# Optimization experiments

Hardware: AMD Instinct MI355X
Metric: run time of the kernel (lower is better)

## Reference

```python
import jax, jax.numpy as jnp
import numpy as np

EPS = 1e-5  # torch GroupNorm default


def setup_inputs() -> dict:
    key = jax.random.key(0)
    ks = jax.random.split(key, 6)
    C = 256
    B, F, H, W = 1, 8, 32, 32
    scale = 1.0 / np.sqrt(C)  # keep logits well-scaled
    return {
        "x": jax.random.normal(ks[0], (B, C, F, H, W), dtype=jnp.float32),
        "gn_w": jnp.ones((C,), jnp.float32),
        "gn_b": jnp.zeros((C,), jnp.float32),
        "qw": jax.random.normal(ks[1], (C, C), jnp.float32) * scale,
        "qb": jnp.zeros((C,), jnp.float32),
        "kw": jax.random.normal(ks[2], (C, C), jnp.float32) * scale,
        "kb": jnp.zeros((C,), jnp.float32),
        "vw": jax.random.normal(ks[3], (C, C), jnp.float32) * scale,
        "vb": jnp.zeros((C,), jnp.float32),
        "ow": jax.random.normal(ks[4], (C, C), jnp.float32) * scale,
        "ob": jnp.zeros((C,), jnp.float32),
    }


def reference(x, gn_w, gn_b, qw, qb, kw, kb, vw, vb, ow, ob):
    B, C, F, H, W = x.shape
    N = F * H * W
    # GroupNorm(1, C): normalize over (C,F,H,W) per sample, per-channel affine
    mean = jnp.mean(x, axis=(1, 2, 3, 4), keepdims=True)
    var = jnp.var(x, axis=(1, 2, 3, 4), keepdims=True)
    xn = (x - mean) * jax.lax.rsqrt(var + EPS)
    xn = xn * gn_w[None, :, None, None, None] + gn_b[None, :, None, None, None]
    xf = xn.reshape(B, C, N)  # [B, C, N]
    # 1x1x1 Conv3d == channel matmul
    q = jnp.einsum('oc,bcn->bon', qw, xf) + qb[None, :, None]
    k = jnp.einsum('oc,bcn->bon', kw, xf) + kb[None, :, None]
    v = jnp.einsum('oc,bcn->bon', vw, xf) + vb[None, :, None]
    # scores[b, n_q, n_k] = q^T k, scaled by C^-0.5
    scores = jnp.einsum('bcn,bcm->bnm', q, k) * (C ** -0.5)
    weights = jax.nn.softmax(scores, axis=-1)  # over keys
    # attention[b, c, n_q] = sum_m v[b,c,m] * weights[b,n_q,m]
    att = jnp.einsum('bcm,bnm->bcn', v, weights)
    att = jnp.einsum('oc,bcn->bon', ow, att) + ob[None, :, None]
    return xn + att.reshape(B, C, F, H, W)
```

## Files before the change

### kernel.cpp

```cpp
#include <hip/hip_runtime.h>
#include <hip/hip_bf16.h>
#include <cstdint>

#define NSP 8192
#define CCH 256
#define KBLK 32
#define NSPLIT 8
#define KEYS_PER_SPLIT 1024
#define NTILES 32

typedef __attribute__((ext_vector_type(4))) float f32x4;
typedef __attribute__((ext_vector_type(16))) float f32x16;
typedef __attribute__((ext_vector_type(8))) short bf16x8;
typedef __attribute__((ext_vector_type(2))) unsigned int u32x2;

__device__ __forceinline__ ushort f2bf(float f) {
  union { float f; uint32_t u; } v; v.f = f;
  uint32_t r = (v.u + 0x7FFFu + ((v.u >> 16) & 1u)) >> 16;
  return (ushort)r;
}
__device__ __forceinline__ float bf2f(ushort u) {
  union { uint32_t u; float f; } v; v.u = ((uint32_t)u) << 16; return v.f;
}
__device__ __forceinline__ uint32_t pk2bf(float lo, float hi) {
  __hip_bfloat162 h = __float22bfloat162_rn({lo, hi});
  union { __hip_bfloat162 h; uint32_t u; } c; c.h = h; return c.u;
}

__device__ __forceinline__ void gload_lds16(const void* g, void* l) {
  auto gp = (const __attribute__((address_space(1))) uint32_t*)(uintptr_t)g;
  auto lp = (__attribute__((address_space(3))) uint32_t*)(uint32_t)(uintptr_t)l;
  __builtin_amdgcn_global_load_lds(gp, lp, 16, 0, 0);
}

__device__ __forceinline__ void perm32swap(uint32_t& a, uint32_t& b) {
#if __has_builtin(__builtin_amdgcn_permlane32_swap)
  u32x2 r = __builtin_amdgcn_permlane32_swap(a, b, false, false);
  a = r[0]; b = r[1];
#else
  uint32_t sa = __shfl_xor((int)a, 32), sb = __shfl_xor((int)b, 32);
  bool lo = (threadIdx.x & 63) < 32;
  uint32_t na = lo ? a : sb;
  uint32_t nb = lo ? sa : b;
  a = na; b = nb;
#endif
}

__global__ __launch_bounds__(256) void k_stats1(const float* __restrict__ x,
                                                float* __restrict__ part) {
  int t = threadIdx.x, b = blockIdx.x;
  float s = 0.f, ss = 0.f;
  const float4* x4 = (const float4*)x;
  for (int i = 0; i < 4; ++i) {
    float4 v = x4[(size_t)i * 131072 + b * 256 + t];
    s += v.x + v.y + v.z + v.w;
    ss += v.x * v.x + v.y * v.y + v.z * v.z + v.w * v.w;
  }
  for (int m = 1; m < 64; m <<= 1) { s += __shfl_xor(s, m); ss += __shfl_xor(ss, m); }
  __shared__ float ls[4], lss[4];
  int w = t >> 6, lane = t & 63;
  if (lane == 0) { ls[w] = s; lss[w] = ss; }
  __syncthreads();
  if (t == 0) {
    part[b * 2 + 0] = ls[0] + ls[1] + ls[2] + ls[3];
    part[b * 2 + 1] = lss[0] + lss[1] + lss[2] + lss[3];
  }
}

__global__ __launch_bounds__(256) void k_castw(const float* __restrict__ qw, const float* __restrict__ kw,
                                               const float* __restrict__ vw, const float* __restrict__ ow,
                                               ushort* __restrict__ wqkv, ushort* __restrict__ wo,
                                               const float* __restrict__ part, float* __restrict__ stat) {
  if (blockIdx.x == 1024) {
    int t = threadIdx.x;
    float s = 0.f, ss = 0.f;
    for (int i = t; i < 512; i += 256) { s += part[i * 2]; ss += part[i * 2 + 1]; }
    for (int m = 1; m < 64; m <<= 1) { s += __shfl_xor(s, m); ss += __shfl_xor(ss, m); }
    __shared__ float ls[4], lss[4];
    int w = t >> 6, lane = t & 63;
    if (lane == 0) { ls[w] = s; lss[w] = ss; }
    __syncthreads();
    if (t == 0) {
      float sum = ls[0] + ls[1] + ls[2] + ls[3];
      float ssum = lss[0] + lss[1] + lss[2] + lss[3];
      float mean = sum * (1.f / 2097152.f);
      float var = ssum * (1.f / 2097152.f) - mean * mean;
      stat[0] = mean;
      stat[1] = rsqrtf(var + 1e-5f);
    }
    return;
  }
  int idx = blockIdx.x * 256 + threadIdx.x;
  if (idx < 65536) wqkv[idx] = f2bf(qw[idx]);
  else if (idx < 131072) wqkv[idx] = f2bf(kw[idx - 65536]);
  else if (idx < 196608) wqkv[idx] = f2bf(vw[idx - 131072]);
  else wo[idx - 196608] = f2bf(ow[idx - 196608]);
}

__global__ __launch_bounds__(256) void k_norm_t(const float* __restrict__ x,
                                                const float* __restrict__ gw, const float* __restrict__ gb,
                                                const float* __restrict__ stat, ushort* __restrict__ xnT) {
  __shared__ float tile[64][66];
  int n0 = blockIdx.x * 64, c0 = blockIdx.y * 64;
  int t = threadIdx.x, colr = t & 63, rq = t >> 6;
  float mean = stat[0], rinv = stat[1];
  for (int rr = 0; rr < 16; ++rr) {
    int row = rr * 4 + rq;
    int c = c0 + row;
    float v = x[(size_t)c * NSP + n0 + colr];
    tile[row][colr] = (v - mean) * rinv * gw[c] + gb[c];
  }
  __syncthreads();
  for (int rr = 0; rr < 16; ++rr) {
    int rowW = rr * 4 + rq;
    xnT[(size_t)(n0 + rowW) * 256 + c0 + colr] = f2bf(tile[colr][rowW]);
  }
}

__global__ __launch_bounds__(256) void k_qkv(const ushort* __restrict__ xnT, const ushort* __restrict__ wqkv,
                                             const float* __restrict__ qb, const float* __restrict__ kb,
                                             const float* __restrict__ vb,
                                             ushort* __restrict__ qT, ushort* __restrict__ kT,
                                             ushort* __restrict__ v_tiles) {
  __shared__ ushort tile[64][80];
  int nb = blockIdx.x, ob = blockIdx.y;
  int w = threadIdx.x >> 6, lane = threadIdx.x & 63;
  int l16 = lane & 15, kgrp = lane >> 4;
  int n_row = nb * 64 + w * 16 + l16;
  bf16x8 a[8];
  const bf16x8* arow = (const bf16x8*)(xnT + (size_t)n_row * 256);
  for (int ks = 0; ks < 8; ++ks) a[ks] = arow[ks * 4 + kgrp];
  f32x4 acc[4];
  for (int ct = 0; ct < 4; ++ct) {
    int o = ob * 64 + ct * 16 + l16;
    const bf16x8* brow = (const bf16x8*)(wqkv + (size_t)o * 256);
    f32x4 c = {0.f, 0.f, 0.f, 0.f};
    for (int ks = 0; ks < 8; ++ks)
      c = __builtin_amdgcn_mfma_f32_16x16x32_bf16(a[ks], brow[ks * 4 + kgrp], c, 0, 0, 0);
    acc[ct] = c;
  }
  const float SCALE = 0.0625f * 1.44269504088896340736f;
  if (ob < 8) {
    for (int ct = 0; ct < 4; ++ct) {
      int o = ob * 64 + ct * 16 + l16;
      for (int r = 0; r < 4; ++r) {
        int n = nb * 64 + w * 16 + kgrp * 4 + r;
        float v = acc[ct][r];
        if (o < 256) qT[(size_t)n * 256 + o] = f2bf((v + qb[o]) * SCALE);
        else kT[(size_t)n * 256 + (o - 256)] = f2bf(v + kb[o - 256]);
      }
    }
  } else {
    for (int ct = 0; ct < 4; ++ct) {
      int o_l = ct * 16 + l16;
      for (int r = 0; r < 4; ++r) {
        int n_l = w * 16 + kgrp * 4 + r;
        tile[o_l][n_l] = f2bf(acc[ct][r] + vb[(ob - 8) * 64 + o_l]);
      }
    }
    __syncthreads();
    for (int j = 0; j < 2; ++j) {
      int idx = j * 256 + threadIdx.x;
      int tile_l = idx >> 8, slot = (idx >> 6) & 3, c_l = idx & 63;
      size_t off = (size_t)(nb * 2 + tile_l) * 8192 + slot * 2048 +
                   (size_t)((ob - 8) * 64 + c_l) * 8;
      *(uint4*)((char*)v_tiles + off * 2) = *(const uint4*)&tile[c_l][tile_l * 32 + slot * 8];
    }
  }
}

__global__ __launch_bounds__(512, 2) void k_attn(const ushort* __restrict__ qT, const ushort* __restrict__ kT,
                                                 const ushort* __restrict__ v_tiles,
                                                 ushort* __restrict__ Opart, float* __restrict__ mpart,
                                                 float* __restrict__ lpart) {
  __shared__ __align__(16) ushort SMEM[32768];
  ushort* k_lds = SMEM;
  ushort* v_lds = SMEM + 16384;

  int bid = blockIdx.x;
  int split = bid & 7, qblk = bid >> 3;
  int t = threadIdx.x, w = t >> 6, lane = t & 63;
  int l31 = lane & 31, lhi = lane >> 5, l7 = lane & 7;
  int q0w = qblk * 256 + w * 32;

  bf16x8 qf[16];
  {
    const char* qbase = (const char*)qT + (size_t)(q0w + l31) * 512;
#pragma unroll
    for (int cs = 0; cs < 16; ++cs)
      qf[cs] = *(const bf16x8*)(qbase + cs * 32 + lhi * 16);
  }

  f32x16 acc[8] = {};
  float m_r = -1e30f, l_p = 0.f;

  const char* kT_b = (const char*)kT + (size_t)split * KEYS_PER_SPLIT * 512;
  const char* v_b = (const char*)v_tiles + (size_t)split * KEYS_PER_SPLIT * 512;

  auto STAGE = [&](int tt, int bsel) {
    const char* ksrc = kT_b + (size_t)tt * KBLK * 512;
    char* kdst = (char*)(k_lds + bsel * 8192) + w * 2048;
#pragma unroll
    for (int i = 0; i < 2; ++i) {
      int keyloc = w * 4 + i * 2 + lhi;
      int srcoff = keyloc * 512 + ((l31 ^ (keyloc & 7)) << 4);
      gload_lds16(ksrc + srcoff, kdst + i * 1024);
    }
    char* vdst = (char*)(v_lds + bsel * 8192) + w * 2048;
    const char* vsrc = v_b + (size_t)tt * 16384 + w * 2048;
#pragma unroll
    for (int i = 0; i < 2; ++i)
      gload_lds16(vsrc + i * 1024 + lane * 16, vdst + i * 1024);
  };

  STAGE(0, 0);

#pragma unroll 1
  for (int tt = 0; tt < NTILES; ++tt) {
    int cur = tt & 1;
    asm volatile("s_waitcnt vmcnt(0) lgkmcnt(0)" ::: "memory");
    __builtin_amdgcn_s_barrier();
    __builtin_amdgcn_sched_barrier(0);
    if (tt + 1 < NTILES) STAGE(tt + 1, cur ^ 1);

    const ushort* kl = k_lds + cur * 8192;
    f32x16 S0 = {};
    __builtin_amdgcn_s_setprio(1);
#pragma unroll
    for (int cs = 0; cs < 16; ++cs) {
      int slot = (cs * 2 + lhi) ^ l7;
      bf16x8 a0 = *(const bf16x8*)(kl + l31 * 256 + slot * 8);
      S0 = __builtin_amdgcn_mfma_f32_32x32x16_bf16(a0, qf[cs], S0, 0, 0, 0);
    }
    __builtin_amdgcn_s_setprio(0);

    float x0 = fmaxf(S0[0], S0[1]), x1 = fmaxf(S0[2], S0[3]);
    float x2 = fmaxf(S0[4], S0[5]), x3 = fmaxf(S0[6], S0[7]);
    float x4 = fmaxf(S0[8], S0[9]), x5 = fmaxf(S0[10], S0[11]);
    float x6 = fmaxf(S0[12], S0[13]), x7 = fmaxf(S0[14], S0[15]);
    float pm = fmaxf(fmaxf(fmaxf(x0, x1), fmaxf(x2, x3)),
                     fmaxf(fmaxf(x4, x5), fmaxf(x6, x7)));
    pm = fmaxf(pm, __shfl_xor(pm, 32));
    if (!__all(pm <= m_r + 8.f)) {
      float mn = fmaxf(m_r, pm);
      float alpha = __builtin_amdgcn_exp2f(m_r - mn);
      m_r = mn;
      l_p *= alpha;
#pragma unroll
      for (int cb = 0; cb < 8; ++cb)
#pragma unroll
        for (int r = 0; r < 16; ++r) acc[cb][r] *= alpha;
    }
    {
      float t0s = 0.f, t1s = 0.f, t2s = 0.f, t3s = 0.f;
#pragma unroll
      for (int r = 0; r < 16; ++r) {
        S0[r] = __builtin_amdgcn_exp2f(S0[r] - m_r);
        if (r < 4) t0s += S0[r];
        else if (r < 8) t1s += S0[r];
        else if (r < 12) t2s += S0[r];
        else t3s += S0[r];
      }
      l_p += (t0s + t1s) + (t2s + t3s);
    }

    bf16x8 pf[2];
    {
      union { uint32_t w[4]; bf16x8 v; } u;
#pragma unroll
      for (int h = 0; h < 2; ++h) {
        int b = h * 8;
        uint32_t x = pk2bf(S0[b + 0], S0[b + 1]), y = pk2bf(S0[b + 4], S0[b + 5]);
        perm32swap(x, y);
        uint32_t x2_ = pk2bf(S0[b + 2], S0[b + 3]), y2 = pk2bf(S0[b + 6], S0[b + 7]);
        perm32swap(x2_, y2);
        u.w[0] = x; u.w[1] = x2_; u.w[2] = y; u.w[3] = y2;
        pf[h] = u.v;
      }
    }

    const ushort* vl = v_lds + cur * 8192;
    __builtin_amdgcn_s_setprio(1);
#pragma unroll
    for (int cb = 0; cb < 8; ++cb) {
#pragma unroll
      for (int h = 0; h < 2; ++h) {
        int s = h * 2 + lhi;
        bf16x8 a = *(const bf16x8*)(vl + s * 2048 + (cb * 32 + l31) * 8);
        acc[cb] = __builtin_amdgcn_mfma_f32_32x32x16_bf16(a, pf[h], acc[cb], 0, 0, 0);
      }
    }
    __builtin_amdgcn_s_setprio(0);
  }

  asm volatile("s_waitcnt vmcnt(0) lgkmcnt(0)" ::: "memory");
  __builtin_amdgcn_s_barrier();

  float l_tot = l_p + __shfl_xor(l_p, 32);

  char* eb = (char*)SMEM + w * 4608;
  size_t gq0 = (size_t)split * NSP + q0w;
#pragma unroll
  for (int ch = 0; ch < 4; ++ch) {
#pragma unroll
    for (int cb2 = 0; cb2 < 2; ++cb2) {
      int cb = ch * 2 + cb2;
#pragma unroll
      for (int g = 0; g < 4; ++g) {
        int cl = cb2 * 32 + g * 8 + 4 * lhi;
        *(uint32_t*)(eb + l31 * 144 + cl * 2) = pk2bf(acc[cb][g * 4 + 0], acc[cb][g * 4 + 1]);
        *(uint32_t*)(eb + l31 * 144 + cl * 2 + 4) = pk2bf(acc[cb][g * 4 + 2], acc[cb][g * 4 + 3]);
      }
    }
    asm volatile("s_waitcnt lgkmcnt(0)" ::: "memory");
    __builtin_amdgcn_sched_barrier(0);
#pragma unroll
    for (int i = 0; i < 4; ++i) {
      int flat = i * 1024 + lane * 16;
      int qr = flat >> 7, off = flat & 127;
      uint4 val = *(const uint4*)(eb + qr * 144 + off);
      *(uint4*)((char*)Opart + (gq0 + qr) * 512 + ch * 128 + off) = val;
    }
    asm volatile("s_waitcnt lgkmcnt(0)" ::: "memory");
    __builtin_amdgcn_sched_barrier(0);
  }
  if (lane < 32) {
    int q = q0w + l31;
    mpart[split * NSP + q] = m_r;
    lpart[split * NSP + q] = l_tot;
  }
}

__global__ __launch_bounds__(256) void k_combine(const ushort* __restrict__ Opart,
                                                 const float* __restrict__ mpart,
                                                 const float* __restrict__ lpart,
                                                 ushort* __restrict__ attT) {
  int q = blockIdx.x;
  int c = threadIdx.x;
  float M = -1e30f;
  for (int s = 0; s < NSPLIT; ++s) M = fmaxf(M, mpart[s * NSP + q]);
  float L = 0.f, acc = 0.f;
  for (int s = 0; s < NSPLIT; ++s) {
    float ws = __builtin_amdgcn_exp2f(mpart[s * NSP + q] - M);
    L += ws * lpart[s * NSP + q];
    acc += ws * bf2f(Opart[((size_t)s * NSP + q) * 256 + c]);
  }
  attT[(size_t)q * 256 + c] = f2bf(acc / L);
}

__global__ __launch_bounds__(256) void k_final(const ushort* __restrict__ attT, const ushort* __restrict__ wo,
                                               const float* __restrict__ ob, const float* __restrict__ x,
                                               const float* __restrict__ gw, const float* __restrict__ gb,
                                               const float* __restrict__ stat, float* __restrict__ out) {
  int nb = blockIdx.x, obk = blockIdx.y;
  int w = threadIdx.x >> 6, lane = threadIdx.x & 63;
  int l16 = lane & 15, kgrp = lane >> 4;
  int orow = obk * 64 + w * 16 + l16;
  bf16x8 a[8];
  const bf16x8* arow = (const bf16x8*)(wo + (size_t)orow * 256);
  for (int ks = 0; ks < 8; ++ks) a[ks] = arow[ks * 4 + kgrp];
  float mean = stat[0], rinv = stat[1];
  f32x4 acc[4];
  for (int ct = 0; ct < 4; ++ct) {
    int n = nb * 64 + ct * 16 + l16;
    const bf16x8* brow = (const bf16x8*)(attT + (size_t)n * 256);
    f32x4 c = {0.f, 0.f, 0.f, 0.f};
    for (int ks = 0; ks < 8; ++ks)
      c = __builtin_amdgcn_mfma_f32_16x16x32_bf16(a[ks], brow[ks * 4 + kgrp], c, 0, 0, 0);
    acc[ct] = c;
  }
  for (int ct = 0; ct < 4; ++ct) {
    for (int r = 0; r < 4; ++r) {
      int o = obk * 64 + w * 16 + kgrp * 4 + r;
      int n = nb * 64 + ct * 16 + l16;
      float xv = x[(size_t)o * NSP + n];
      float xn = (xv - mean) * rinv * gw[o] + gb[o];
      out[(size_t)o * NSP + n] = xn + acc[ct][r] + ob[o];
    }
  }
}

extern "C" void kernel_launch(void* const* d_in, const int* in_sizes, int n_in,
                              void* d_out, int out_size, void* d_ws, size_t ws_size,
                              hipStream_t stream) {
  const float* x = (const float*)d_in[0];
  const float* gw = (const float*)d_in[1];
  const float* gb = (const float*)d_in[2];
  const float* qw = (const float*)d_in[3];
  const float* qbv = (const float*)d_in[4];
  const float* kw = (const float*)d_in[5];
  const float* kbv = (const float*)d_in[6];
  const float* vw = (const float*)d_in[7];
  const float* vbv = (const float*)d_in[8];
  const float* ow = (const float*)d_in[9];
  const float* obv = (const float*)d_in[10];
  float* out = (float*)d_out;
  char* ws = (char*)d_ws;
  const size_t KB = 1024, MB = 1048576;
  float* part = (float*)(ws);
  float* stat = (float*)(ws + 60 * KB);
  ushort* wqkv = (ushort*)(ws + 64 * KB);
  ushort* wo = (ushort*)(ws + 448 * KB);
  float* mpart = (float*)(ws + 64 * KB);
  float* lpart = (float*)(ws + 576 * KB);
  ushort* xnT = (ushort*)(ws + 1 * MB);
  ushort* qT = (ushort*)(ws + 5 * MB);
  ushort* kT = (ushort*)(ws + 9 * MB);
  ushort* v_tiles = (ushort*)(ws + 13 * MB);
  ushort* Opart = (ushort*)(ws + 17 * MB);
  ushort* attT = xnT;

  k_stats1<<<512, 256, 0, stream>>>(x, part);
  k_castw<<<1025, 256, 0, stream>>>(qw, kw, vw, ow, wqkv, wo, part, stat);
  k_norm_t<<<dim3(128, 4), 256, 0, stream>>>(x, gw, gb, stat, xnT);
  k_qkv<<<dim3(128, 12), 256, 0, stream>>>(xnT, wqkv, qbv, kbv, vbv, qT, kT, v_tiles);
  k_attn<<<256, 512, 0, stream>>>(qT, kT, v_tiles, Opart, mpart, lpart);
  k_combine<<<NSP, 256, 0, stream>>>(Opart, mpart, lpart, attT);
  k_final<<<dim3(128, 4), 256, 0, stream>>>(attT, wo, obv, x, gw, gb, stat, out);
}
```

Measured before the change: 145.6 us.

## Software-pipeline attention loop: interleave QK of next tile with PV of previous

Restructures the flash-attention main loop so that the QK^T MFMAs for tile tt are interleaved with the P·V MFMAs for tile tt-1. K and V staging are split so K is prefetched one tile ahead and V is loaded one tile behind. A prologue computes the first score tile and an epilogue runs the final PV. The goal is to break the serial dependency chain of the 16 score MFMAs and hide it behind the independent accumulate MFMAs. In exchange the loop carries more live registers and has more complex buffer indexing.

```diff
diff --git a/kernel.cpp b/kernel.cpp
--- a/kernel.cpp
+++ b/kernel.cpp
@@ -193,47 +193,30 @@
 
   f32x16 acc[8] = {};
   float m_r = -1e30f, l_p = 0.f;
+  bf16x8 pf0, pf1;
 
   const char* kT_b = (const char*)kT + (size_t)split * KEYS_PER_SPLIT * 512;
   const char* v_b = (const char*)v_tiles + (size_t)split * KEYS_PER_SPLIT * 512;
 
-  auto STAGE = [&](int tt, int bsel) {
+  auto STAGE_K = [&](int tt) {
     const char* ksrc = kT_b + (size_t)tt * KBLK * 512;
-    char* kdst = (char*)(k_lds + bsel * 8192) + w * 2048;
+    char* kdst = (char*)(k_lds + (tt & 1) * 8192) + w * 2048;
 #pragma unroll
     for (int i = 0; i < 2; ++i) {
       int keyloc = w * 4 + i * 2 + lhi;
       int srcoff = keyloc * 512 + ((l31 ^ (keyloc & 7)) << 4);
       gload_lds16(ksrc + srcoff, kdst + i * 1024);
     }
-    char* vdst = (char*)(v_lds + bsel * 8192) + w * 2048;
+  };
+  auto STAGE_V = [&](int tt) {
+    char* vdst = (char*)(v_lds + (tt & 1) * 8192) + w * 2048;
     const char* vsrc = v_b + (size_t)tt * 16384 + w * 2048;
 #pragma unroll
     for (int i = 0; i < 2; ++i)
       gload_lds16(vsrc + i * 1024 + lane * 16, vdst + i * 1024);
   };
 
-  STAGE(0, 0);
-
-#pragma unroll 1
-  for (int tt = 0; tt < NTILES; ++tt) {
-    int cur = tt & 1;
-    asm volatile("s_waitcnt vmcnt(0) lgkmcnt(0)" ::: "memory");
-    __builtin_amdgcn_s_barrier();
-    __builtin_amdgcn_sched_barrier(0);
-    if (tt + 1 < NTILES) STAGE(tt + 1, cur ^ 1);
-
-    const ushort* kl = k_lds + cur * 8192;
-    f32x16 S0 = {};
-    __builtin_amdgcn_s_setprio(1);
-#pragma unroll
-    for (int cs = 0; cs < 16; ++cs) {
-      int slot = (cs * 2 + lhi) ^ l7;
-      bf16x8 a0 = *(const bf16x8*)(kl + l31 * 256 + slot * 8);
-      S0 = __builtin_amdgcn_mfma_f32_32x32x16_bf16(a0, qf[cs], S0, 0, 0, 0);
-    }
-    __builtin_amdgcn_s_setprio(0);
-
+  auto SOFTMAX_PACK = [&](f32x16& S0) {
     float x0 = fmaxf(S0[0], S0[1]), x1 = fmaxf(S0[2], S0[3]);
     float x2 = fmaxf(S0[4], S0[5]), x3 = fmaxf(S0[6], S0[7]);
     float x4 = fmaxf(S0[8], S0[9]), x5 = fmaxf(S0[10], S0[11]);
@@ -263,37 +246,97 @@
       }
       l_p += (t0s + t1s) + (t2s + t3s);
     }
-
-    bf16x8 pf[2];
+    union { uint32_t w[4]; bf16x8 v; } u;
     {
-      union { uint32_t w[4]; bf16x8 v; } u;
-#pragma unroll
-      for (int h = 0; h < 2; ++h) {
-        int b = h * 8;
-        uint32_t x = pk2bf(S0[b + 0], S0[b + 1]), y = pk2bf(S0[b + 4], S0[b + 5]);
-        perm32swap(x, y);
-        uint32_t x2_ = pk2bf(S0[b + 2], S0[b + 3]), y2 = pk2bf(S0[b + 6], S0[b + 7]);
-        perm32swap(x2_, y2);
-        u.w[0] = x; u.w[1] = x2_; u.w[2] = y; u.w[3] = y2;
-        pf[h] = u.v;
-      }
-    }
-
-    const ushort* vl = v_lds + cur * 8192;
+      uint32_t x = pk2bf(S0[0], S0[1]), y = pk2bf(S0[4], S0[5]);
+      perm32swap(x, y);
+      uint32_t x2_ = pk2bf(S0[2], S0[3]), y2 = pk2bf(S0[6], S0[7]);
+      perm32swap(x2_, y2);
+      u.w[0] = x; u.w[1] = x2_; u.w[2] = y; u.w[3] = y2;
+      pf0 = u.v;
+    }
+    {
+      uint32_t x = pk2bf(S0[8], S0[9]), y = pk2bf(S0[12], S0[13]);
+      perm32swap(x, y);
+      uint32_t x2_ = pk2bf(S0[10], S0[11]), y2 = pk2bf(S0[14], S0[15]);
+      perm32swap(x2_, y2);
+      u.w[0] = x; u.w[1] = x2_; u.w[2] = y; u.w[3] = y2;
+      pf1 = u.v;
+    }
+  };
+
+  STAGE_K(0);
+
+  asm volatile("s_waitcnt vmcnt(0) lgkmcnt(0)" ::: "memory");
+  __builtin_amdgcn_s_barrier();
+  __builtin_amdgcn_sched_barrier(0);
+  STAGE_K(1);
+  STAGE_V(0);
+  {
+    const ushort* kl = k_lds;
+    f32x16 S0 = {};
     __builtin_amdgcn_s_setprio(1);
 #pragma unroll
+    for (int cs = 0; cs < 16; ++cs) {
+      int slot = (cs * 2 + lhi) ^ l7;
+      bf16x8 a0 = *(const bf16x8*)(kl + l31 * 256 + slot * 8);
+      S0 = __builtin_amdgcn_mfma_f32_32x32x16_bf16(a0, qf[cs], S0, 0, 0, 0);
+    }
+    __builtin_amdgcn_s_setprio(0);
+    SOFTMAX_PACK(S0);
+  }
+
+#pragma unroll 1
+  for (int tt = 1; tt < NTILES; ++tt) {
+    asm volatile("s_waitcnt vmcnt(0) lgkmcnt(0)" ::: "memory");
+    __builtin_amdgcn_s_barrier();
+    __builtin_amdgcn_sched_barrier(0);
+    if (tt + 1 < NTILES) STAGE_K(tt + 1);
+    STAGE_V(tt);
+
+    const ushort* kl = k_lds + (tt & 1) * 8192;
+    const ushort* vl = v_lds + ((tt - 1) & 1) * 8192;
+    f32x16 S0 = {};
+    __builtin_amdgcn_s_setprio(1);
+#pragma unroll
     for (int cb = 0; cb < 8; ++cb) {
-#pragma unroll
-      for (int h = 0; h < 2; ++h) {
-        int s = h * 2 + lhi;
-        bf16x8 a = *(const bf16x8*)(vl + s * 2048 + (cb * 32 + l31) * 8);
-        acc[cb] = __builtin_amdgcn_mfma_f32_32x32x16_bf16(a, pf[h], acc[cb], 0, 0, 0);
+      bf16x8 va0 = *(const bf16x8*)(vl + (0 + lhi) * 2048 + (cb * 32 + l31) * 8);
+      acc[cb] = __builtin_amdgcn_mfma_f32_32x32x16_bf16(va0, pf0, acc[cb], 0, 0, 0);
+      {
+        int cs = 2 * cb;
+        int slot = (cs * 2 + lhi) ^ l7;
+        bf16x8 ka = *(const bf16x8*)(kl + l31 * 256 + slot * 8);
+        S0 = __builtin_amdgcn_mfma_f32_32x32x16_bf16(ka, qf[cs], S0, 0, 0, 0);
+      }
+      bf16x8 va1 = *(const bf16x8*)(vl + (2 + lhi) * 2048 + (cb * 32 + l31) * 8);
+      acc[cb] = __builtin_amdgcn_mfma_f32_32x32x16_bf16(va1, pf1, acc[cb], 0, 0, 0);
+      {
+        int cs = 2 * cb + 1;
+        int slot = (cs * 2 + lhi) ^ l7;
+        bf16x8 ka = *(const bf16x8*)(kl + l31 * 256 + slot * 8);
+        S0 = __builtin_amdgcn_mfma_f32_32x32x16_bf16(ka, qf[cs], S0, 0, 0, 0);
       }
     }
     __builtin_amdgcn_s_setprio(0);
+    SOFTMAX_PACK(S0);
   }
 
   asm volatile("s_waitcnt vmcnt(0) lgkmcnt(0)" ::: "memory");
+  __builtin_amdgcn_s_barrier();
+  {
+    const ushort* vl = v_lds + ((NTILES - 1) & 1) * 8192;
+    __builtin_amdgcn_s_setprio(1);
+#pragma unroll
+    for (int cb = 0; cb < 8; ++cb) {
+      bf16x8 va0 = *(const bf16x8*)(vl + (0 + lhi) * 2048 + (cb * 32 + l31) * 8);
+      acc[cb] = __builtin_amdgcn_mfma_f32_32x32x16_bf16(va0, pf0, acc[cb], 0, 0, 0);
+      bf16x8 va1 = *(const bf16x8*)(vl + (2 + lhi) * 2048 + (cb * 32 + l31) * 8);
+      acc[cb] = __builtin_amdgcn_mfma_f32_32x32x16_bf16(va1, pf1, acc[cb], 0, 0, 0);
+    }
+    __builtin_amdgcn_s_setprio(0);
+  }
+
+  asm volatile("s_waitcnt lgkmcnt(0)" ::: "memory");
   __builtin_amdgcn_s_barrier();
 
   float l_tot = l_p + __shfl_xor(l_p, 32);
```

After: 140.7 us. 3.4% less time.
